# Kernel optimization log

Hardware: AMD Instinct MI355X
Metric: run time of the kernel (lower is better)

Reference implementation:

```python
import jax, jax.numpy as jnp
import numpy as np

B, T, C, H = 4, 2048, 1024, 16
D = C // H
EPS = 1e-5


def setup_inputs() -> dict:
    key = jax.random.key(0)
    ks = jax.random.split(key, 8)
    s = 0.02
    return {
        "hidden_states": jax.random.normal(ks[0], (B, T, C), jnp.float32),
        "w_attn": jax.random.normal(ks[1], (C, 3 * C), jnp.float32) * s,
        "b_attn": jnp.zeros((3 * C,), jnp.float32),
        "w_proj": jax.random.normal(ks[2], (C, C), jnp.float32) * s,
        "b_proj": jnp.zeros((C,), jnp.float32),
        "ln1_g": jnp.ones((C,), jnp.float32),
        "ln1_b": jnp.zeros((C,), jnp.float32),
        "ln2_g": jnp.ones((C,), jnp.float32),
        "ln2_b": jnp.zeros((C,), jnp.float32),
        "w_fc": jax.random.normal(ks[3], (C, 4 * C), jnp.float32) * s,
        "b_fc": jnp.zeros((4 * C,), jnp.float32),
        "w_fc2": jax.random.normal(ks[4], (4 * C, C), jnp.float32) * s,
        "b_fc2": jnp.zeros((C,), jnp.float32),
    }


def _layernorm(x, g, b):
    mu = jnp.mean(x, axis=-1, keepdims=True)
    var = jnp.mean(jnp.square(x - mu), axis=-1, keepdims=True)
    return (x - mu) * jax.lax.rsqrt(var + EPS) * g + b


def _attention(x, w_attn, b_attn, w_proj, b_proj):
    Bx, Tx, Cx = x.shape
    qkv = x @ w_attn + b_attn  # [B,T,3C]  (GCLinear transpose=True => x @ W)
    q, k, v = jnp.split(qkv, 3, axis=-1)
    # [B,T,C] -> [B,H,T,D]
    q = q.reshape(Bx, Tx, H, D).transpose(0, 2, 1, 3)
    k = k.reshape(Bx, Tx, H, D).transpose(0, 2, 1, 3)
    v = v.reshape(Bx, Tx, H, D).transpose(0, 2, 1, 3)
    att = jnp.einsum("bhqd,bhkd->bhqk", q, k) * (1.0 / np.sqrt(D))
    causal = jnp.tril(jnp.ones((Tx, Tx), bool))
    att = jnp.where(causal, att, -jnp.inf)
    att = jax.nn.softmax(att, axis=-1)
    y = jnp.einsum("bhqk,bhkd->bhqd", att, v)
    y = y.transpose(0, 2, 1, 3).reshape(Bx, Tx, Cx)
    return y @ w_proj + b_proj


def reference(hidden_states, w_attn, b_attn, w_proj, b_proj,
              ln1_g, ln1_b, ln2_g, ln2_b, w_fc, b_fc, w_fc2, b_fc2):
    x = hidden_states
    a = _attention(_layernorm(x, ln1_g, ln1_b), w_attn, b_attn, w_proj, b_proj)
    x = x + a
    h = _layernorm(x, ln2_g, ln2_b)
    h = jax.nn.gelu(h @ w_fc + b_fc, approximate=False)  # nn.GELU default = exact erf
    h = h @ w_fc2 + b_fc2
    return x + h
```

## Files before the change

### kernel.cpp

```cpp
#include <hip/hip_runtime.h>
#include <hip/hip_bf16.h>
#include <stdint.h>

typedef __bf16 bf16_t;
typedef __bf16 bf16x8 __attribute__((ext_vector_type(8)));
typedef __bf16 bf16x4 __attribute__((ext_vector_type(4)));
typedef float f32x4 __attribute__((ext_vector_type(4)));
typedef short short4v __attribute__((ext_vector_type(4)));

#define BDIM_B 4
#define TDIM 2048
#define CDIM 1024

__device__ __forceinline__ void gload16(const void* g, void* l) {
  using GP = const __attribute__((address_space(1))) char*;
  using LP = __attribute__((address_space(3))) char*;
  __builtin_amdgcn_global_load_lds((GP)(uintptr_t)g, (LP)(uint32_t)(uintptr_t)l, 16, 0, 0);
}

__global__ __launch_bounds__(256)
void transpose_cast(const float* __restrict__ W, bf16_t* __restrict__ Wt, int K, int N) {
  __shared__ float tile[32][33];
  const int tx = threadIdx.x & 31, ty = threadIdx.x >> 5;
  const int n0 = blockIdx.x * 32, k0 = blockIdx.y * 32;
#pragma unroll
  for (int j = 0; j < 32; j += 8)
    tile[ty + j][tx] = W[(size_t)(k0 + ty + j) * N + n0 + tx];
  __syncthreads();
#pragma unroll
  for (int j = 0; j < 32; j += 8)
    Wt[(size_t)(n0 + ty + j) * K + k0 + tx] = (bf16_t)tile[tx][ty + j];
}

__global__ __launch_bounds__(256)
void ln_kernel(const float* __restrict__ x, const float* __restrict__ g,
               const float* __restrict__ bta, bf16_t* __restrict__ out) {
  const size_t row = blockIdx.x;
  const int tid = threadIdx.x;
  const float4 v = ((const float4*)(x + row * CDIM))[tid];
  float s = v.x + v.y + v.z + v.w;
#pragma unroll
  for (int off = 1; off < 64; off <<= 1) s += __shfl_xor(s, off);
  __shared__ float r1[4], r2[4];
  const int wv = tid >> 6, lane = tid & 63;
  if (!lane) r1[wv] = s;
  __syncthreads();
  const float mu = (r1[0] + r1[1] + r1[2] + r1[3]) * (1.f / CDIM);
  const float dx = v.x - mu, dy = v.y - mu, dz = v.z - mu, dw = v.w - mu;
  float q = dx * dx + dy * dy + dz * dz + dw * dw;
#pragma unroll
  for (int off = 1; off < 64; off <<= 1) q += __shfl_xor(q, off);
  if (!lane) r2[wv] = q;
  __syncthreads();
  const float var = (r2[0] + r2[1] + r2[2] + r2[3]) * (1.f / CDIM);
  const float rs = rsqrtf(var + 1e-5f);
  const float4 gg = ((const float4*)g)[tid];
  const float4 bb = ((const float4*)bta)[tid];
  bf16x4 o;
  o[0] = (bf16_t)(dx * rs * gg.x + bb.x);
  o[1] = (bf16_t)(dy * rs * gg.y + bb.y);
  o[2] = (bf16_t)(dz * rs * gg.z + bb.z);
  o[3] = (bf16_t)(dw * rs * gg.w + bb.w);
  ((bf16x4*)(out + row * CDIM))[tid] = o;
}

enum { EPI_BF16 = 0, EPI_RESID = 1, EPI_GELU = 2 };

template <int EPI>
__global__ __launch_bounds__(256)
void gemm_bt(const bf16_t* __restrict__ A, const bf16_t* __restrict__ Bt,
             const float* __restrict__ bias, const float* __restrict__ resid,
             void* __restrict__ outv, int M, int N, int K) {
  __shared__ bf16_t tA[128 * 32];
  __shared__ bf16_t tB[128 * 32];
  const int tid = threadIdx.x;
  const int lane = tid & 63;
  const int wv = tid >> 6;
  const int wr = wv >> 1, wc = wv & 1;
  const int rin = lane & 15, quad = lane >> 4;
  const int m0 = blockIdx.y * 128, n0 = blockIdx.x * 128;
  const int srow = lane >> 2, sseg = lane & 3;

  f32x4 acc[4][4] = {};

  for (int kt = 0; kt < K; kt += 32) {
    __syncthreads();
#pragma unroll
    for (int t = 0; t < 2; ++t) {
      const int inst = t * 4 + wv;
      const int row = inst * 16 + srow;
      gload16(A + (size_t)(m0 + row) * K + kt + sseg * 8, tA + inst * 512);
      gload16(Bt + (size_t)(n0 + row) * K + kt + sseg * 8, tB + inst * 512);
    }
    __syncthreads();
    bf16x8 af[4], bf[4];
#pragma unroll
    for (int i = 0; i < 4; ++i)
      af[i] = *(const bf16x8*)(tA + (wr * 64 + i * 16 + rin) * 32 + quad * 8);
#pragma unroll
    for (int i = 0; i < 4; ++i)
      bf[i] = *(const bf16x8*)(tB + (wc * 64 + i * 16 + rin) * 32 + quad * 8);
#pragma unroll
    for (int mi = 0; mi < 4; ++mi)
#pragma unroll
      for (int ni = 0; ni < 4; ++ni)
        acc[mi][ni] = __builtin_amdgcn_mfma_f32_16x16x32_bf16(af[mi], bf[ni], acc[mi][ni], 0, 0, 0);
  }

  const int rbase = m0 + wr * 64 + quad * 4;
  const int cbase = n0 + wc * 64 + rin;
#pragma unroll
  for (int mi = 0; mi < 4; ++mi)
#pragma unroll
    for (int ni = 0; ni < 4; ++ni)
#pragma unroll
      for (int r = 0; r < 4; ++r) {
        const int m = rbase + mi * 16 + r;
        const int n = cbase + ni * 16;
        float v = acc[mi][ni][r] + bias[n];
        if (EPI == EPI_RESID) v += resid[(size_t)m * N + n];
        if (EPI == EPI_GELU) v = 0.5f * v * (1.0f + erff(v * 0.7071067811865476f));
        if (EPI == EPI_RESID)
          ((float*)outv)[(size_t)m * N + n] = v;
        else
          ((bf16_t*)outv)[(size_t)m * N + n] = (bf16_t)v;
      }
}

__global__ __launch_bounds__(256)
void attn_kernel(const bf16_t* __restrict__ qkv, bf16_t* __restrict__ y) {
  const int h = blockIdx.y, b = blockIdx.z;
  const int tid = threadIdx.x, lane = tid & 63, wv = tid >> 6;
  const int rin = lane & 15, quad = lane >> 4;

  __shared__ bf16_t Kt[64 * 64];
  __shared__ bf16_t Vt[64 * 64];

  const size_t base3 = (size_t)(b * TDIM) * 3072;
  const int srow = tid >> 2, sseg = tid & 3;
  const short4v ones = {(short)0x3F80, (short)0x3F80, (short)0x3F80, (short)0x3F80};

#pragma unroll 1
  for (int seg = 0; seg < 2; ++seg) {
    const int qt = seg ? blockIdx.x : (15 - blockIdx.x);
    const int q0 = qt * 128;
    const int nkt = qt * 2 + 2;

    bf16x8 aq[2][2];
#pragma unroll
    for (int qf = 0; qf < 2; ++qf) {
      const size_t qr = base3 + (size_t)(q0 + wv * 32 + qf * 16 + rin) * 3072 + h * 64;
#pragma unroll
      for (int ki = 0; ki < 2; ++ki)
        aq[qf][ki] = *(const bf16x8*)(qkv + qr + ki * 32 + quad * 8);
    }

    uint4 kreg[2], vreg[2];
#pragma unroll
    for (int hf = 0; hf < 2; ++hf) {
      const size_t gb = base3 + (size_t)srow * 3072 + h * 64 + hf * 32 + sseg * 8;
      kreg[hf] = *(const uint4*)(qkv + gb + 1024);
      vreg[hf] = *(const uint4*)(qkv + gb + 2048);
    }

    f32x4 o[2][4] = {};
    f32x4 ol[2] = {};

    for (int kt = 0; kt < nkt; ++kt) {
      __syncthreads();
      {
        const int krot = (srow >> 2) & 7;
        const int tg = srow >> 3, to = srow & 7;
#pragma unroll
        for (int hf = 0; hf < 2; ++hf) {
          const int g = hf * 4 + sseg;
          *(uint4*)(Kt + srow * 64 + (((g + krot) & 7) * 8)) = kreg[hf];
          union { uint4 u; bf16_t e[8]; } vv;
          vv.u = vreg[hf];
#pragma unroll
          for (int j = 0; j < 8; ++j) {
            const int d = hf * 32 + sseg * 8 + j;
            Vt[d * 64 + (((tg + ((d >> 2) & 7)) & 7) * 8) + to] = vv.e[j];
          }
        }
      }
      __syncthreads();
      {
        const int ktn = (kt + 1 < nkt) ? kt + 1 : kt;
#pragma unroll
        for (int hf = 0; hf < 2; ++hf) {
          const size_t gb = base3 + (size_t)(ktn * 64 + srow) * 3072 + h * 64 + hf * 32 + sseg * 8;
          kreg[hf] = *(const uint4*)(qkv + gb + 1024);
          vreg[hf] = *(const uint4*)(qkv + gb + 2048);
        }
      }
      f32x4 st[2][4] = {};
#pragma unroll
      for (int ki = 0; ki < 2; ++ki) {
        bf16x8 ak[4];
#pragma unroll
        for (int kf = 0; kf < 4; ++kf) {
          const int tr = kf * 16 + rin;
          ak[kf] = *(const bf16x8*)(Kt + tr * 64 + (((ki * 4 + quad + ((tr >> 2) & 7)) & 7) * 8));
        }
#pragma unroll
        for (int qf = 0; qf < 2; ++qf)
#pragma unroll
          for (int kf = 0; kf < 4; ++kf)
            st[qf][kf] = __builtin_amdgcn_mfma_f32_16x16x32_bf16(ak[kf], aq[qf][ki], st[qf][kf], 0, 0, 0);
      }
      const bool maskt = (kt >= 2 * qt);
      short4v pf[2][4];
#pragma unroll
      for (int qf = 0; qf < 2; ++qf) {
        const int qg = q0 + wv * 32 + qf * 16 + rin;
#pragma unroll
        for (int kf = 0; kf < 4; ++kf)
#pragma unroll
          for (int r = 0; r < 4; ++r) {
            const int kg = kt * 64 + kf * 16 + quad * 4 + r;
            float p = __builtin_amdgcn_exp2f(st[qf][kf][r] * 0.18033688f);
            if (maskt && kg > qg) p = 0.f;
            union { bf16_t bv; short sv; } cv;
            cv.bv = (bf16_t)p;
            pf[qf][kf][r] = cv.sv;
          }
      }
#pragma unroll
      for (int kf = 0; kf < 4; ++kf) {
        short4v bv[4];
#pragma unroll
        for (int nd = 0; nd < 4; ++nd) {
          const int d = nd * 16 + rin;
          const int sw = (2 * kf + (quad >> 1) + ((d >> 2) & 7)) & 7;
          bv[nd] = *(const short4v*)(Vt + d * 64 + sw * 8 + (quad & 1) * 4);
        }
#pragma unroll
        for (int qf = 0; qf < 2; ++qf) {
#pragma unroll
          for (int nd = 0; nd < 4; ++nd)
            o[qf][nd] = __builtin_amdgcn_mfma_f32_16x16x16bf16_1k(pf[qf][kf], bv[nd], o[qf][nd], 0, 0, 0);
          ol[qf] = __builtin_amdgcn_mfma_f32_16x16x16bf16_1k(pf[qf][kf], ones, ol[qf], 0, 0, 0);
        }
      }
    }

#pragma unroll
    for (int qf = 0; qf < 2; ++qf)
#pragma unroll
      for (int r = 0; r < 4; ++r) {
        const float inv = 1.0f / ol[qf][r];
        const size_t row = (size_t)b * TDIM + q0 + wv * 32 + qf * 16 + quad * 4 + r;
#pragma unroll
        for (int nd = 0; nd < 4; ++nd)
          y[row * CDIM + h * 64 + nd * 16 + rin] = (bf16_t)(o[qf][nd][r] * inv);
      }
  }
}

extern "C" void kernel_launch(void* const* d_in, const int* in_sizes, int n_in,
                              void* d_out, int out_size, void* d_ws, size_t ws_size,
                              hipStream_t stream) {
  const float* x      = (const float*)d_in[0];
  const float* w_attn = (const float*)d_in[1];
  const float* b_attn = (const float*)d_in[2];
  const float* w_proj = (const float*)d_in[3];
  const float* b_proj = (const float*)d_in[4];
  const float* ln1g   = (const float*)d_in[5];
  const float* ln1b   = (const float*)d_in[6];
  const float* ln2g   = (const float*)d_in[7];
  const float* ln2b   = (const float*)d_in[8];
  const float* w_fc   = (const float*)d_in[9];
  const float* b_fc   = (const float*)d_in[10];
  const float* w_fc2  = (const float*)d_in[11];
  const float* b_fc2  = (const float*)d_in[12];
  float* out = (float*)d_out;

  char* ws = (char*)d_ws;
  bf16_t* wTattn = (bf16_t*)(ws + 0);
  bf16_t* wTproj = (bf16_t*)(ws + 6291456);
  bf16_t* wTfc   = (bf16_t*)(ws + 8388608);
  bf16_t* wTfc2  = (bf16_t*)(ws + 16777216);
  bf16_t* xn     = (bf16_t*)(ws + 25165824);
  float*  x2     = (float*)(ws + 41943040);
  bf16_t* qkv    = (bf16_t*)(ws + 75497472);
  bf16_t* yb     = (bf16_t*)(ws + 75497472 + 50331648);
  bf16_t* hb     = (bf16_t*)(ws + 75497472);

  transpose_cast<<<dim3(96, 32), 256, 0, stream>>>(w_attn, wTattn, 1024, 3072);
  transpose_cast<<<dim3(32, 32), 256, 0, stream>>>(w_proj, wTproj, 1024, 1024);
  transpose_cast<<<dim3(128, 32), 256, 0, stream>>>(w_fc, wTfc, 1024, 4096);
  transpose_cast<<<dim3(32, 128), 256, 0, stream>>>(w_fc2, wTfc2, 4096, 1024);

  ln_kernel<<<8192, 256, 0, stream>>>(x, ln1g, ln1b, xn);
  gemm_bt<EPI_BF16><<<dim3(24, 64), 256, 0, stream>>>(xn, wTattn, b_attn, nullptr, qkv, 8192, 3072, 1024);
  attn_kernel<<<dim3(8, 16, 4), 256, 0, stream>>>(qkv, yb);
  gemm_bt<EPI_RESID><<<dim3(8, 64), 256, 0, stream>>>(yb, wTproj, b_proj, x, x2, 8192, 1024, 1024);
  ln_kernel<<<8192, 256, 0, stream>>>(x2, ln2g, ln2b, xn);
  gemm_bt<EPI_GELU><<<dim3(32, 64), 256, 0, stream>>>(xn, wTfc, b_fc, nullptr, hb, 8192, 4096, 1024);
  gemm_bt<EPI_RESID><<<dim3(8, 64), 256, 0, stream>>>(hb, wTfc2, b_fc2, x2, out, 8192, 1024, 4096);
}
```

Measured before the change: 578.8 us.

## Replace GEMM with 256x256 double-buffered, swizzled, pipelined MFMA kernel

```diff
diff --git a/kernel.cpp b/kernel.cpp
--- a/kernel.cpp
+++ b/kernel.cpp
@@ -67,50 +67,114 @@
 enum { EPI_BF16 = 0, EPI_RESID = 1, EPI_GELU = 2 };
 
 template <int EPI>
-__global__ __launch_bounds__(256)
-void gemm_bt(const bf16_t* __restrict__ A, const bf16_t* __restrict__ Bt,
+__global__ __launch_bounds__(512)
+void gemm256(const bf16_t* __restrict__ A, const bf16_t* __restrict__ Bt,
              const float* __restrict__ bias, const float* __restrict__ resid,
              void* __restrict__ outv, int M, int N, int K) {
-  __shared__ bf16_t tA[128 * 32];
-  __shared__ bf16_t tB[128 * 32];
+  __shared__ bf16_t sA[2][256 * 64];
+  __shared__ bf16_t sB[2][256 * 64];
   const int tid = threadIdx.x;
-  const int lane = tid & 63;
-  const int wv = tid >> 6;
-  const int wr = wv >> 1, wc = wv & 1;
+  const int lane = tid & 63, wv = tid >> 6;
+  const int wm = wv >> 2, wn = wv & 3;
   const int rin = lane & 15, quad = lane >> 4;
-  const int m0 = blockIdx.y * 128, n0 = blockIdx.x * 128;
-  const int srow = lane >> 2, sseg = lane & 3;
-
-  f32x4 acc[4][4] = {};
-
-  for (int kt = 0; kt < K; kt += 32) {
-    __syncthreads();
-#pragma unroll
-    for (int t = 0; t < 2; ++t) {
-      const int inst = t * 4 + wv;
-      const int row = inst * 16 + srow;
-      gload16(A + (size_t)(m0 + row) * K + kt + sseg * 8, tA + inst * 512);
-      gload16(Bt + (size_t)(n0 + row) * K + kt + sseg * 8, tB + inst * 512);
-    }
-    __syncthreads();
-    bf16x8 af[4], bf[4];
-#pragma unroll
-    for (int i = 0; i < 4; ++i)
-      af[i] = *(const bf16x8*)(tA + (wr * 64 + i * 16 + rin) * 32 + quad * 8);
-#pragma unroll
-    for (int i = 0; i < 4; ++i)
-      bf[i] = *(const bf16x8*)(tB + (wc * 64 + i * 16 + rin) * 32 + quad * 8);
-#pragma unroll
-    for (int mi = 0; mi < 4; ++mi)
-#pragma unroll
-      for (int ni = 0; ni < 4; ++ni)
-        acc[mi][ni] = __builtin_amdgcn_mfma_f32_16x16x32_bf16(af[mi], bf[ni], acc[mi][ni], 0, 0, 0);
+
+  const int nwg = gridDim.x * gridDim.y;
+  const int bid = blockIdx.y * gridDim.x + blockIdx.x;
+  const int swzb = (bid & 7) * (nwg >> 3) + (bid >> 3);
+  const int bx = swzb % gridDim.x, by = swzb / gridDim.x;
+  const int m0 = by * 256, n0 = bx * 256;
+
+  const int c8 = (lane & 7) ^ ((lane >> 3) & 7);
+  const int aRow = wm * 128 + (wv & 3) * 8 + (lane >> 3);
+  const int bRow = wn * 64 + (wv >> 2) * 8 + (lane >> 3);
+  const bf16_t* srcA = A + (size_t)(m0 + aRow) * K + c8 * 8;
+  const bf16_t* srcB = Bt + (size_t)(n0 + bRow) * K + c8 * 8;
+  const int dstA = (wm * 128 + (wv & 3) * 8) * 64;
+  const int dstB = (wn * 64 + (wv >> 2) * 8) * 64;
+
+#define STA(buf, r, kk) gload16(srcA + (size_t)(32 * (r)) * K + (kk), (buf) + dstA + 32 * (r) * 64)
+#define STB(buf, r, kk) gload16(srcB + (size_t)(16 * (r)) * K + (kk), (buf) + dstB + 16 * (r) * 64)
+
+  const int ck0 = (quad ^ (rin & 7)) * 8;
+  const int ck1 = ((4 + quad) ^ (rin & 7)) * 8;
+  const int aBase = (wm * 128 + rin) * 64;
+  const int bBase = (wn * 64 + rin) * 64;
+
+  f32x4 acc[8][4] = {};
+  bf16x8 af[8][2], bfr[4][2];
+
+#define RDA(mi) { af[mi][0] = *(const bf16x8*)(rA + aBase + (mi)*1024 + ck0); \
+                  af[mi][1] = *(const bf16x8*)(rA + aBase + (mi)*1024 + ck1); }
+#define RDB(ni) { bfr[ni][0] = *(const bf16x8*)(rB + bBase + (ni)*1024 + ck0); \
+                  bfr[ni][1] = *(const bf16x8*)(rB + bBase + (ni)*1024 + ck1); }
+#define MM(mi, ni) { acc[mi][ni] = __builtin_amdgcn_mfma_f32_16x16x32_bf16(af[mi][0], bfr[ni][0], acc[mi][ni], 0, 0, 0); \
+                     acc[mi][ni] = __builtin_amdgcn_mfma_f32_16x16x32_bf16(af[mi][1], bfr[ni][1], acc[mi][ni], 0, 0, 0); }
+
+  const int NT = K >> 6;
+
+  {
+    bf16_t* wA = sA[0];
+    bf16_t* wB = sB[0];
+    STA(wA, 0, 0); STB(wB, 0, 0); STB(wB, 1, 0);
+    STA(wA, 1, 0); STB(wB, 2, 0); STB(wB, 3, 0);
+    STA(wA, 2, 0);
+    STA(wA, 3, 0);
   }
 
-  const int rbase = m0 + wr * 64 + quad * 4;
-  const int cbase = n0 + wc * 64 + rin;
-#pragma unroll
-  for (int mi = 0; mi < 4; ++mi)
+  for (int t = 0; t < NT; ++t) {
+    const bf16_t* rA = sA[t & 1];
+    const bf16_t* rB = sB[t & 1];
+    bf16_t* wA = sA[(t & 1) ^ 1];
+    bf16_t* wB = sB[(t & 1) ^ 1];
+    const int kk = (t + 1 < NT ? t + 1 : t) * 64;
+
+    asm volatile("s_waitcnt vmcnt(5)" ::: "memory");
+    __builtin_amdgcn_s_barrier();
+    __builtin_amdgcn_sched_barrier(0);
+    RDA(0) RDA(1) RDB(0) RDB(1)
+    STA(wA, 0, kk); STB(wB, 0, kk); STB(wB, 1, kk);
+    __builtin_amdgcn_s_setprio(1);
+    MM(0, 0) MM(0, 1) MM(1, 0) MM(1, 1)
+    __builtin_amdgcn_s_setprio(0);
+    __builtin_amdgcn_sched_barrier(0);
+
+    asm volatile("s_waitcnt vmcnt(5)" ::: "memory");
+    __builtin_amdgcn_s_barrier();
+    __builtin_amdgcn_sched_barrier(0);
+    RDA(2) RDA(3) RDB(2) RDB(3)
+    STA(wA, 1, kk); STB(wB, 2, kk); STB(wB, 3, kk);
+    __builtin_amdgcn_s_setprio(1);
+    MM(0, 2) MM(0, 3) MM(1, 2) MM(1, 3) MM(2, 0) MM(2, 1) MM(3, 0) MM(3, 1)
+    __builtin_amdgcn_s_setprio(0);
+    __builtin_amdgcn_sched_barrier(0);
+
+    asm volatile("s_waitcnt vmcnt(7)" ::: "memory");
+    __builtin_amdgcn_s_barrier();
+    __builtin_amdgcn_sched_barrier(0);
+    RDA(4) RDA(5)
+    STA(wA, 2, kk);
+    __builtin_amdgcn_s_setprio(1);
+    MM(2, 2) MM(2, 3) MM(3, 2) MM(3, 3) MM(4, 0) MM(4, 1) MM(5, 0) MM(5, 1)
+    __builtin_amdgcn_s_setprio(0);
+    __builtin_amdgcn_sched_barrier(0);
+
+    asm volatile("s_waitcnt vmcnt(7)" ::: "memory");
+    __builtin_amdgcn_s_barrier();
+    __builtin_amdgcn_sched_barrier(0);
+    RDA(6) RDA(7)
+    STA(wA, 3, kk);
+    __builtin_amdgcn_s_setprio(1);
+    MM(4, 2) MM(4, 3) MM(5, 2) MM(5, 3) MM(6, 0) MM(6, 1) MM(7, 0) MM(7, 1)
+    MM(6, 2) MM(6, 3) MM(7, 2) MM(7, 3)
+    __builtin_amdgcn_s_setprio(0);
+    __builtin_amdgcn_sched_barrier(0);
+  }
+  asm volatile("s_waitcnt vmcnt(0)" ::: "memory");
+
+  const int rbase = m0 + wm * 128 + quad * 4;
+  const int cbase = n0 + wn * 64 + rin;
+#pragma unroll
+  for (int mi = 0; mi < 8; ++mi)
 #pragma unroll
     for (int ni = 0; ni < 4; ++ni)
 #pragma unroll
@@ -125,6 +189,11 @@
         else
           ((bf16_t*)outv)[(size_t)m * N + n] = (bf16_t)v;
       }
+#undef STA
+#undef STB
+#undef RDA
+#undef RDB
+#undef MM
 }
 
 __global__ __launch_bounds__(256)
@@ -293,10 +362,10 @@
   transpose_cast<<<dim3(32, 128), 256, 0, stream>>>(w_fc2, wTfc2, 4096, 1024);
 
   ln_kernel<<<8192, 256, 0, stream>>>(x, ln1g, ln1b, xn);
-  gemm_bt<EPI_BF16><<<dim3(24, 64), 256, 0, stream>>>(xn, wTattn, b_attn, nullptr, qkv, 8192, 3072, 1024);
+  gemm256<EPI_BF16><<<dim3(12, 32), 512, 0, stream>>>(xn, wTattn, b_attn, nullptr, qkv, 8192, 3072, 1024);
   attn_kernel<<<dim3(8, 16, 4), 256, 0, stream>>>(qkv, yb);
-  gemm_bt<EPI_RESID><<<dim3(8, 64), 256, 0, stream>>>(yb, wTproj, b_proj, x, x2, 8192, 1024, 1024);
+  gemm256<EPI_RESID><<<dim3(4, 32), 512, 0, stream>>>(yb, wTproj, b_proj, x, x2, 8192, 1024, 1024);
   ln_kernel<<<8192, 256, 0, stream>>>(x2, ln2g, ln2b, xn);
-  gemm_bt<EPI_GELU><<<dim3(32, 64), 256, 0, stream>>>(xn, wTfc, b_fc, nullptr, hb, 8192, 4096, 1024);
-  gemm_bt<EPI_RESID><<<dim3(8, 64), 256, 0, stream>>>(hb, wTfc2, b_fc2, x2, out, 8192, 1024, 4096);
-}
+  gemm256<EPI_GELU><<<dim3(16, 32), 512, 0, stream>>>(xn, wTfc, b_fc, nullptr, hb, 8192, 4096, 1024);
+  gemm256<EPI_RESID><<<dim3(4, 32), 512, 0, stream>>>(hb, wTfc2, b_fc2, x2, out, 8192, 1024, 4096);
+}
```

After: 550.2 us. 1.05x faster.
